# Performance work log

Measured on AMD Instinct MI355X. Metric: run time of the kernel, lower is better.

## Reference

```python
import jax, jax.numpy as jnp
import numpy as np

SEQ_LEN = 8192
DIM_AUD = 2048
NEG_SLOPE = 0.02


def _leaky(z):
    return jnp.where(z >= 0, z, NEG_SLOPE * z)


def _conv1d(x, w, b):
    # x: [1, Cin, L], w: [Cout, Cin, 3], b: [Cout]; stride 1, padding 1
    y = jax.lax.conv_general_dilated(
        x, w, window_strides=(1,), padding=[(1, 1)],
        dimension_numbers=('NCH', 'OIH', 'NCH'))
    return y + b[None, :, None]


def setup_inputs() -> dict:
    key = jax.random.key(0)
    ks = jax.random.split(key, 13)
    def rn(k, shape, fan_in):
        return jax.random.normal(k, shape, dtype=jnp.float32) * (1.0 / np.sqrt(fan_in))
    x = jax.random.normal(ks[0], (SEQ_LEN, DIM_AUD), dtype=jnp.float32)
    w1 = rn(ks[1], (16, DIM_AUD, 3), DIM_AUD * 3); b1 = jnp.zeros((16,), jnp.float32)
    w2 = rn(ks[2], (8, 16, 3), 16 * 3);            b2 = jnp.zeros((8,), jnp.float32)
    w3 = rn(ks[3], (4, 8, 3), 8 * 3);              b3 = jnp.zeros((4,), jnp.float32)
    w4 = rn(ks[4], (2, 4, 3), 4 * 3);              b4 = jnp.zeros((2,), jnp.float32)
    w5 = rn(ks[5], (1, 2, 3), 2 * 3);              b5 = jnp.zeros((1,), jnp.float32)
    Wl = rn(ks[6], (SEQ_LEN, SEQ_LEN), SEQ_LEN);   bl = jnp.zeros((SEQ_LEN,), jnp.float32)
    return {"x": x, "w1": w1, "b1": b1, "w2": w2, "b2": b2, "w3": w3, "b3": b3,
            "w4": w4, "b4": b4, "w5": w5, "b5": b5, "Wl": Wl, "bl": bl}


def reference(x, w1, b1, w2, b2, w3, b3, w4, b4, w5, b5, Wl, bl):
    # y: [1, dim_aud, seq_len]
    y = x[:, :DIM_AUD].T[None]
    y = _leaky(_conv1d(y, w1, b1))
    y = _leaky(_conv1d(y, w2, b2))
    y = _leaky(_conv1d(y, w3, b3))
    y = _leaky(_conv1d(y, w4, b4))
    y = _leaky(_conv1d(y, w5, b5))          # [1, 1, seq_len]
    logits = y.reshape(1, SEQ_LEN) @ Wl.T + bl  # torch Linear: x @ W.T + b
    att = jax.nn.softmax(logits, axis=1).reshape(SEQ_LEN, 1)
    return jnp.sum(att * x, axis=0)          # [dim_aud]
```

## Files before the change

kernel.cpp:

```cpp
#include <hip/hip_runtime.h>

#define SEQ 8192
#define DIM 2048
#define NEG 0.02f

__global__ __launch_bounds__(256, 2) void k_conv1(
    const float* __restrict__ x, const float* __restrict__ w1,
    float* __restrict__ out1p) {
  __shared__ float wlds[32 * 16 * 12];
  __shared__ float xs[32 * 260];

  const int tid = threadIdx.x;
  const int tb = blockIdx.x & 31;
  const int slice = blockIdx.x >> 5;
  const int cinb = slice * 128;

  for (int i = tid; i < 6144; i += 256) {
    int c = i / 384;
    int rem = i - c * 384;
    int uu = rem / 3;
    int k = rem - uu * 3;
    float v = w1[c * 6144 + (cinb + uu) * 3 + k];
    wlds[((uu >> 2) * 16 + c) * 12 + k * 4 + (uu & 3)] = v;
  }

  const int cg = tid & 3;
  const int tg = tid >> 2;
  const int qc = tid & 7;
  const int rs = tid >> 3;

  float acc[4][4];
  #pragma unroll
  for (int i = 0; i < 4; ++i)
    #pragma unroll
    for (int tt = 0; tt < 4; ++tt) acc[i][tt] = 0.f;

  const float4* x4 = (const float4*)x;

  for (int ch = 0; ch < 4; ++ch) {
    __syncthreads();
    #pragma unroll
    for (int it = 0; it < 9; ++it) {
      int r = rs + it * 32;
      if (r < 258) {
        int gt = tb * 256 - 1 + r;
        float4 v = make_float4(0.f, 0.f, 0.f, 0.f);
        if (gt >= 0 && gt < SEQ)
          v = x4[gt * 512 + (cinb >> 2) + ch * 8 + qc];
        xs[(4 * qc + 0) * 260 + r] = v.x;
        xs[(4 * qc + 1) * 260 + r] = v.y;
        xs[(4 * qc + 2) * 260 + r] = v.z;
        xs[(4 * qc + 3) * 260 + r] = v.w;
      }
    }
    __syncthreads();

    #pragma unroll 1
    for (int gg = 0; gg < 8; ++gg) {
      const float4* wp = (const float4*)&wlds[(ch * 8 + gg) * 16 * 12];
      float4 wk[4][3];
      #pragma unroll
      for (int i = 0; i < 4; ++i)
        #pragma unroll
        for (int k = 0; k < 3; ++k)
          wk[i][k] = wp[(4 * cg + i) * 3 + k];
      const float* wkf = (const float*)wk;

      #pragma unroll
      for (int u = 0; u < 4; ++u) {
        const float* xb = &xs[(gg * 4 + u) * 260 + 4 * tg];
        float4 xa = *(const float4*)xb;
        float2 xt = *(const float2*)(xb + 4);
        float xv[6] = {xa.x, xa.y, xa.z, xa.w, xt.x, xt.y};
        #pragma unroll
        for (int i = 0; i < 4; ++i) {
          #pragma unroll
          for (int k = 0; k < 3; ++k) {
            float wv = wkf[(i * 3 + k) * 4 + u];
            #pragma unroll
            for (int tt = 0; tt < 4; ++tt)
              acc[i][tt] += wv * xv[tt + k];
          }
        }
      }
    }
  }

  #pragma unroll
  for (int i = 0; i < 4; ++i) {
    float4 o = make_float4(acc[i][0], acc[i][1], acc[i][2], acc[i][3]);
    int c = 4 * cg + i;
    ((float4*)out1p)[(slice * 16 + c) * 2048 + tb * 64 + tg] = o;
  }
}

__global__ __launch_bounds__(128) void k_chain(
    const float* __restrict__ out1p, const float* __restrict__ b1,
    const float* __restrict__ w2, const float* __restrict__ b2,
    const float* __restrict__ w3, const float* __restrict__ b3,
    const float* __restrict__ w4, const float* __restrict__ b4,
    const float* __restrict__ w5, const float* __restrict__ b5,
    float* __restrict__ y5) {
  __shared__ float l1[16][72], l2[8][72], l3[4][72], l4[2][72];
  __shared__ float w2s[384], w3s[96], w4s[24], w5s[6];
  __shared__ float bs[16];

  const int tid = threadIdx.x;
  const int t0 = blockIdx.x * 64;

  for (int i = tid; i < 384; i += 128) w2s[i] = w2[i];
  if (tid < 96) w3s[tid] = w3[tid];
  else if (tid < 120) w4s[tid - 96] = w4[tid - 96];
  else if (tid == 120) { for (int i = 0; i < 6; ++i) w5s[i] = w5[i]; }
  else if (tid == 121) {
    for (int i = 0; i < 8; ++i) bs[i] = b2[i];
    for (int i = 0; i < 4; ++i) bs[8 + i] = b3[i];
    bs[12] = b4[0]; bs[13] = b4[1]; bs[14] = b5[0];
  }

  const float4* p4 = (const float4*)out1p;
  for (int idx = tid; idx < 16 * 18; idx += 128) {
    int cc = idx / 18, m = idx - cc * 18;
    int gt0 = t0 - 4 + 4 * m;
    float4 a = make_float4(0.f, 0.f, 0.f, 0.f);
    if (gt0 >= 0 && gt0 < SEQ) {
      int base = cc * 2048 + (gt0 >> 2);
      #pragma unroll
      for (int s = 0; s < 16; ++s) {
        float4 v = p4[s * 16 * 2048 + base];
        a.x += v.x; a.y += v.y; a.z += v.z; a.w += v.w;
      }
    }
    float bb = b1[cc];
    float e0 = a.x + bb, e1 = a.y + bb, e2 = a.z + bb, e3 = a.w + bb;
    l1[cc][4 * m + 0] = (e0 >= 0.f) ? e0 : NEG * e0;
    l1[cc][4 * m + 1] = (e1 >= 0.f) ? e1 : NEG * e1;
    l1[cc][4 * m + 2] = (e2 >= 0.f) ? e2 : NEG * e2;
    l1[cc][4 * m + 3] = (e3 >= 0.f) ? e3 : NEG * e3;
  }
  __syncthreads();

  for (int o = tid; o < 560; o += 128) {
    int j = (o >> 3) + 1, cc = o & 7;
    float acc = bs[cc];
    #pragma unroll
    for (int ci = 0; ci < 16; ++ci) {
      acc += w2s[cc * 48 + ci * 3 + 0] * l1[ci][j - 1];
      acc += w2s[cc * 48 + ci * 3 + 1] * l1[ci][j];
      acc += w2s[cc * 48 + ci * 3 + 2] * l1[ci][j + 1];
    }
    l2[cc][j] = (acc >= 0.f) ? acc : NEG * acc;
  }
  __syncthreads();

  for (int o = tid; o < 272; o += 128) {
    int j = (o >> 2) + 2, cc = o & 3;
    float acc = bs[8 + cc];
    #pragma unroll
    for (int ci = 0; ci < 8; ++ci) {
      acc += w3s[cc * 24 + ci * 3 + 0] * l2[ci][j - 1];
      acc += w3s[cc * 24 + ci * 3 + 1] * l2[ci][j];
      acc += w3s[cc * 24 + ci * 3 + 2] * l2[ci][j + 1];
    }
    l3[cc][j] = (acc >= 0.f) ? acc : NEG * acc;
  }
  __syncthreads();

  for (int o = tid; o < 132; o += 128) {
    int j = (o >> 1) + 3, cc = o & 1;
    float acc = bs[12 + cc];
    #pragma unroll
    for (int ci = 0; ci < 4; ++ci) {
      acc += w4s[cc * 12 + ci * 3 + 0] * l3[ci][j - 1];
      acc += w4s[cc * 12 + ci * 3 + 1] * l3[ci][j];
      acc += w4s[cc * 12 + ci * 3 + 2] * l3[ci][j + 1];
    }
    l4[cc][j] = (acc >= 0.f) ? acc : NEG * acc;
  }
  __syncthreads();

  for (int o = tid; o < 64; o += 128) {
    int j = o + 4;
    float acc = bs[14];
    #pragma unroll
    for (int ci = 0; ci < 2; ++ci) {
      acc += w5s[ci * 3 + 0] * l4[ci][j - 1];
      acc += w5s[ci * 3 + 1] * l4[ci][j];
      acc += w5s[ci * 3 + 2] * l4[ci][j + 1];
    }
    y5[t0 + o] = (acc >= 0.f) ? acc : NEG * acc;
  }
}

__global__ __launch_bounds__(256) void k_matvec(
    const float* __restrict__ Wl, const float* __restrict__ bl,
    const float* __restrict__ y5, float* __restrict__ logits) {
  const int tid = threadIdx.x;
  const int r0 = blockIdx.x * 8;
  const float4* W4 = (const float4*)Wl;
  const float4* y4 = (const float4*)y5;

  float a[8];
  #pragma unroll
  for (int r = 0; r < 8; ++r) a[r] = 0.f;

  #pragma unroll 2
  for (int u = 0; u < 8; ++u) {
    int i = u * 256 + tid;
    float4 yv = y4[i];
    #pragma unroll
    for (int r = 0; r < 8; ++r) {
      float4 wv = W4[(r0 + r) * 2048 + i];
      a[r] += wv.x * yv.x + wv.y * yv.y + wv.z * yv.z + wv.w * yv.w;
    }
  }
  #pragma unroll
  for (int o = 32; o; o >>= 1) {
    #pragma unroll
    for (int r = 0; r < 8; ++r) a[r] += __shfl_down(a[r], o);
  }
  __shared__ float red[4][8];
  const int lane = tid & 63, wid = tid >> 6;
  if (lane == 0) {
    #pragma unroll
    for (int r = 0; r < 8; ++r) red[wid][r] = a[r];
  }
  __syncthreads();
  if (tid < 8) {
    float s = red[0][tid] + red[1][tid] + red[2][tid] + red[3][tid];
    logits[r0 + tid] = s + bl[r0 + tid];
  }
}

__global__ __launch_bounds__(256) void k_stats(
    const float* __restrict__ logits, float* __restrict__ stats) {
  __shared__ float red[4];
  const int tid = threadIdx.x;
  const int lane = tid & 63, wid = tid >> 6;

  float lv[32];
  #pragma unroll
  for (int i = 0; i < 32; ++i) lv[i] = logits[tid + 256 * i];

  float m = lv[0];
  #pragma unroll
  for (int i = 1; i < 32; ++i) m = fmaxf(m, lv[i]);
  #pragma unroll
  for (int o = 32; o; o >>= 1) m = fmaxf(m, __shfl_down(m, o));
  if (lane == 0) red[wid] = m;
  __syncthreads();
  const float M = fmaxf(fmaxf(red[0], red[1]), fmaxf(red[2], red[3]));
  __syncthreads();

  float s = 0.f;
  #pragma unroll
  for (int i = 0; i < 32; ++i) s += __expf(lv[i] - M);
  #pragma unroll
  for (int o = 32; o; o >>= 1) s += __shfl_down(s, o);
  if (lane == 0) red[wid] = s;
  __syncthreads();
  if (tid == 0) {
    float S = red[0] + red[1] + red[2] + red[3];
    stats[0] = M;
    stats[1] = 1.0f / S;
  }
}

__global__ __launch_bounds__(256) void k_wsum(
    const float* __restrict__ x, const float* __restrict__ logits,
    const float* __restrict__ stats, float* __restrict__ partial) {
  const int tid = threadIdx.x;
  const int lane = tid & 63, wv = tid >> 6;
  const int tc = blockIdx.x >> 3, strip = blockIdx.x & 7;
  const float M = stats[0], invS = stats[1];
  const float4* x4 = (const float4*)x;
  const int col = strip * 64 + lane;
  const int t0 = tc * 64 + wv * 16;

  float4 acc = make_float4(0.f, 0.f, 0.f, 0.f);
  #pragma unroll 4
  for (int tt = 0; tt < 16; ++tt) {
    int t = t0 + tt;
    float a = __expf(logits[t] - M) * invS;
    float4 xv = x4[t * 512 + col];
    acc.x += a * xv.x; acc.y += a * xv.y; acc.z += a * xv.z; acc.w += a * xv.w;
  }

  __shared__ float4 redx[4][64];
  redx[wv][lane] = acc;
  __syncthreads();
  if (wv == 0) {
    float4 s = redx[0][lane];
    #pragma unroll
    for (int w = 1; w < 4; ++w) {
      float4 v = redx[w][lane];
      s.x += v.x; s.y += v.y; s.z += v.z; s.w += v.w;
    }
    ((float4*)partial)[tc * 512 + col] = s;
  }
}

__global__ __launch_bounds__(256) void k_reduce(
    const float* __restrict__ partial, float* __restrict__ out) {
  const int col = blockIdx.x * 256 + threadIdx.x;
  float s = 0.f;
  #pragma unroll 8
  for (int tc = 0; tc < 128; ++tc) s += partial[tc * 2048 + col];
  out[col] = s;
}

extern "C" void kernel_launch(void* const* d_in, const int* in_sizes, int n_in,
                              void* d_out, int out_size, void* d_ws, size_t ws_size,
                              hipStream_t stream) {
  const float* x  = (const float*)d_in[0];
  const float* w1 = (const float*)d_in[1];
  const float* b1 = (const float*)d_in[2];
  const float* w2 = (const float*)d_in[3];
  const float* b2 = (const float*)d_in[4];
  const float* w3 = (const float*)d_in[5];
  const float* b3 = (const float*)d_in[6];
  const float* w4 = (const float*)d_in[7];
  const float* b4 = (const float*)d_in[8];
  const float* w5 = (const float*)d_in[9];
  const float* b5 = (const float*)d_in[10];
  const float* Wl = (const float*)d_in[11];
  const float* bl = (const float*)d_in[12];
  float* out = (float*)d_out;

  float* ws      = (float*)d_ws;
  float* out1p   = ws;
  float* y5      = out1p + 16 * 16 * SEQ;
  float* logits  = y5 + SEQ;
  float* stats   = logits + SEQ;
  float* partial = stats + 16;

  k_conv1 <<<512, 256, 0, stream>>>(x, w1, out1p);
  k_chain <<<128, 128, 0, stream>>>(out1p, b1, w2, b2, w3, b3, w4, b4, w5, b5, y5);
  k_matvec<<<1024, 256, 0, stream>>>(Wl, bl, y5, logits);
  k_stats <<<1, 256, 0, stream>>>(logits, stats);
  k_wsum  <<<1024, 256, 0, stream>>>(x, logits, stats, partial);
  k_reduce<<<8, 256, 0, stream>>>(partial, out);
}
```

Before: 118.3 us.

## Pre-transpose conv1 weights and read them wave-uniformly from global memory

Adds a small prep kernel that repacks w1 into a [cin][cout] float4 layout, so each conv1 block no longer builds a weight tile in LDS. The conv1 thread mapping changes so each wave owns four output channels, which makes the weight loads wave-uniform and lets them come from scalar or cached global reads. The x tile in LDS gets per-row padding to avoid bank conflicts. The cost is an extra kernel launch and weight reads from global or L2 inside the inner loop.

After: 140.3 us. +18.6%, slower.

```diff
diff --git a/kernel.cpp b/kernel.cpp
--- a/kernel.cpp
+++ b/kernel.cpp
@@ -4,30 +4,35 @@
 #define DIM 2048
 #define NEG 0.02f
 
+__global__ __launch_bounds__(256) void k_prep(
+    const float* __restrict__ w1, float* __restrict__ wT) {
+  int i = blockIdx.x * 256 + threadIdx.x;
+  if (i < 32768) {
+    int cin = i >> 4, c = i & 15;
+    const float* s = w1 + c * 6144 + cin * 3;
+    ((float4*)wT)[i] = make_float4(s[0], s[1], s[2], 0.f);
+  }
+}
+
+__device__ __forceinline__ int row_off(int j) {
+  return j * 260 + (j >> 2) * 4;
+}
+
 __global__ __launch_bounds__(256, 2) void k_conv1(
-    const float* __restrict__ x, const float* __restrict__ w1,
+    const float* __restrict__ x, const float* __restrict__ wT,
     float* __restrict__ out1p) {
-  __shared__ float wlds[32 * 16 * 12];
-  __shared__ float xs[32 * 260];
+  __shared__ float xs[8348];
 
   const int tid = threadIdx.x;
   const int tb = blockIdx.x & 31;
   const int slice = blockIdx.x >> 5;
-  const int cinb = slice * 128;
-
-  for (int i = tid; i < 6144; i += 256) {
-    int c = i / 384;
-    int rem = i - c * 384;
-    int uu = rem / 3;
-    int k = rem - uu * 3;
-    float v = w1[c * 6144 + (cinb + uu) * 3 + k];
-    wlds[((uu >> 2) * 16 + c) * 12 + k * 4 + (uu & 3)] = v;
-  }
-
-  const int cg = tid & 3;
-  const int tg = tid >> 2;
+  const int cinb = slice << 7;
+  const int lane = tid & 63;
+  const int wv = __builtin_amdgcn_readfirstlane(tid >> 6);
+  const int t0 = tb << 8;
   const int qc = tid & 7;
   const int rs = tid >> 3;
+  const float4* x4 = (const float4*)x;
 
   float acc[4][4];
   #pragma unroll
@@ -35,53 +40,44 @@
     #pragma unroll
     for (int tt = 0; tt < 4; ++tt) acc[i][tt] = 0.f;
 
-  const float4* x4 = (const float4*)x;
+  const float* xrow = xs + (lane << 2);
 
   for (int ch = 0; ch < 4; ++ch) {
     __syncthreads();
     #pragma unroll
     for (int it = 0; it < 9; ++it) {
-      int r = rs + it * 32;
+      int r = rs + (it << 5);
       if (r < 258) {
-        int gt = tb * 256 - 1 + r;
+        int gt = t0 - 1 + r;
         float4 v = make_float4(0.f, 0.f, 0.f, 0.f);
         if (gt >= 0 && gt < SEQ)
-          v = x4[gt * 512 + (cinb >> 2) + ch * 8 + qc];
-        xs[(4 * qc + 0) * 260 + r] = v.x;
-        xs[(4 * qc + 1) * 260 + r] = v.y;
-        xs[(4 * qc + 2) * 260 + r] = v.z;
-        xs[(4 * qc + 3) * 260 + r] = v.w;
+          v = x4[gt * 512 + (cinb >> 2) + (ch << 3) + qc];
+        xs[row_off(4 * qc + 0) + r] = v.x;
+        xs[row_off(4 * qc + 1) + r] = v.y;
+        xs[row_off(4 * qc + 2) + r] = v.z;
+        xs[row_off(4 * qc + 3) + r] = v.w;
       }
     }
     __syncthreads();
 
-    #pragma unroll 1
-    for (int gg = 0; gg < 8; ++gg) {
-      const float4* wp = (const float4*)&wlds[(ch * 8 + gg) * 16 * 12];
-      float4 wk[4][3];
+    const float4* wq = ((const float4*)wT) + (((cinb + (ch << 5)) << 4) + (wv << 2));
+
+    #pragma unroll 8
+    for (int cin = 0; cin < 32; ++cin) {
+      float4 w0 = wq[(cin << 4) + 0];
+      float4 w1v = wq[(cin << 4) + 1];
+      float4 w2v = wq[(cin << 4) + 2];
+      float4 w3v = wq[(cin << 4) + 3];
+      const float* xb = xrow + row_off(cin);
+      float4 xa = *(const float4*)xb;
+      float2 xt = *(const float2*)(xb + 4);
+      float xv[6] = {xa.x, xa.y, xa.z, xa.w, xt.x, xt.y};
       #pragma unroll
-      for (int i = 0; i < 4; ++i)
-        #pragma unroll
-        for (int k = 0; k < 3; ++k)
-          wk[i][k] = wp[(4 * cg + i) * 3 + k];
-      const float* wkf = (const float*)wk;
-
-      #pragma unroll
-      for (int u = 0; u < 4; ++u) {
-        const float* xb = &xs[(gg * 4 + u) * 260 + 4 * tg];
-        float4 xa = *(const float4*)xb;
-        float2 xt = *(const float2*)(xb + 4);
-        float xv[6] = {xa.x, xa.y, xa.z, xa.w, xt.x, xt.y};
-        #pragma unroll
-        for (int i = 0; i < 4; ++i) {
-          #pragma unroll
-          for (int k = 0; k < 3; ++k) {
-            float wv = wkf[(i * 3 + k) * 4 + u];
-            #pragma unroll
-            for (int tt = 0; tt < 4; ++tt)
-              acc[i][tt] += wv * xv[tt + k];
-          }
-        }
+      for (int tt = 0; tt < 4; ++tt) {
+        acc[0][tt] += w0.x * xv[tt] + w0.y * xv[tt + 1] + w0.z * xv[tt + 2];
+        acc[1][tt] += w1v.x * xv[tt] + w1v.y * xv[tt + 1] + w1v.z * xv[tt + 2];
+        acc[2][tt] += w2v.x * xv[tt] + w2v.y * xv[tt + 1] + w2v.z * xv[tt + 2];
+        acc[3][tt] += w3v.x * xv[tt] + w3v.y * xv[tt + 1] + w3v.z * xv[tt + 2];
       }
     }
   }
@@ -89,8 +85,8 @@
   #pragma unroll
   for (int i = 0; i < 4; ++i) {
     float4 o = make_float4(acc[i][0], acc[i][1], acc[i][2], acc[i][3]);
-    int c = 4 * cg + i;
-    ((float4*)out1p)[(slice * 16 + c) * 2048 + tb * 64 + tg] = o;
+    int c = (wv << 2) + i;
+    ((float4*)out1p)[(slice * 16 + c) * 2048 + (t0 >> 2) + lane] = o;
   }
 }
 
@@ -328,13 +324,15 @@
   float* out = (float*)d_out;
 
   float* ws      = (float*)d_ws;
-  float* out1p   = ws;
+  float* wT      = ws;
+  float* out1p   = wT + 131072;
   float* y5      = out1p + 16 * 16 * SEQ;
   float* logits  = y5 + SEQ;
   float* stats   = logits + SEQ;
   float* partial = stats + 16;
 
-  k_conv1 <<<512, 256, 0, stream>>>(x, w1, out1p);
+  k_prep  <<<128, 256, 0, stream>>>(w1, wT);
+  k_conv1 <<<512, 256, 0, stream>>>(x, wT, out1p);
   k_chain <<<128, 128, 0, stream>>>(out1p, b1, w2, b2, w3, b3, w4, b4, w5, b5, y5);
   k_matvec<<<1024, 256, 0, stream>>>(Wl, bl, y5, logits);
   k_stats <<<1, 256, 0, stream>>>(logits, stats);
```

## Retile conv1 with wave-uniform output channels and padded LDS rows

Applied to the files above, without the earlier changes.

The first convolution is retiled so each block covers 512 time steps and 64 input channels, and each wave owns 4 output channels. Weights become wave-uniform, and each thread computes 8 time points. LDS rows get periodic padding to reduce bank conflicts, and the three taps are folded into one expression. The trade-off is twice as many partial slices (32 instead of 16), so the chain kernel reads a larger partial buffer and the workspace grows. Out-of-range halo entries in the chain kernel are now written as zero instead of leaky(bias).

Result: slower. 136.7 us (+15.5%).

```diff
diff --git a/kernel.cpp b/kernel.cpp
--- a/kernel.cpp
+++ b/kernel.cpp
@@ -4,82 +4,90 @@
 #define DIM 2048
 #define NEG 0.02f
 
+__device__ __forceinline__ int row_off(int j) {
+  return j * 520 + (j >> 2) * 4;
+}
+
 __global__ __launch_bounds__(256, 2) void k_conv1(
     const float* __restrict__ x, const float* __restrict__ w1,
     float* __restrict__ out1p) {
-  __shared__ float wlds[32 * 16 * 12];
-  __shared__ float xs[32 * 260];
-
-  const int tid = threadIdx.x;
-  const int tb = blockIdx.x & 31;
-  const int slice = blockIdx.x >> 5;
-  const int cinb = slice * 128;
-
-  for (int i = tid; i < 6144; i += 256) {
-    int c = i / 384;
-    int rem = i - c * 384;
-    int uu = rem / 3;
-    int k = rem - uu * 3;
-    float v = w1[c * 6144 + (cinb + uu) * 3 + k];
-    wlds[((uu >> 2) * 16 + c) * 12 + k * 4 + (uu & 3)] = v;
-  }
-
-  const int cg = tid & 3;
-  const int tg = tid >> 2;
-  const int qc = tid & 7;
-  const int rs = tid >> 3;
-
-  float acc[4][4];
+  __shared__ float wlds[16 * 16 * 12];
+  __shared__ float xs[8332];
+
+  const int tid = threadIdx.x;
+  const int tb = blockIdx.x & 15;
+  const int slice = blockIdx.x >> 4;
+  const int cinb = slice << 6;
+  const int lane = tid & 63;
+  const int wv = __builtin_amdgcn_readfirstlane(tid >> 6);
+  const int t0 = tb << 9;
+  const float4* x4 = (const float4*)x;
+
+  for (int i = tid; i < 3072; i += 256) {
+    int g = i / 192;
+    int rem = i - g * 192;
+    int c = rem / 12;
+    int m = rem - c * 12;
+    int k = m >> 2, u = m & 3;
+    wlds[i] = w1[c * 6144 + (cinb + 4 * g + u) * 3 + k];
+  }
+
+  float acc[4][8];
   #pragma unroll
   for (int i = 0; i < 4; ++i)
     #pragma unroll
-    for (int tt = 0; tt < 4; ++tt) acc[i][tt] = 0.f;
-
-  const float4* x4 = (const float4*)x;
+    for (int t = 0; t < 8; ++t) acc[i][t] = 0.f;
+
+  const int qc = tid & 3;
+  const int rsb = tid >> 2;
 
   for (int ch = 0; ch < 4; ++ch) {
     __syncthreads();
     #pragma unroll
     for (int it = 0; it < 9; ++it) {
-      int r = rs + it * 32;
-      if (r < 258) {
-        int gt = tb * 256 - 1 + r;
+      int srr = rsb + (it << 6);
+      if (srr < 516) {
+        int region = (srr >= 258) ? 1 : 0;
+        int rr = srr - 258 * region;
+        int gt = t0 - 1 + rr + (region << 8);
         float4 v = make_float4(0.f, 0.f, 0.f, 0.f);
         if (gt >= 0 && gt < SEQ)
-          v = x4[gt * 512 + (cinb >> 2) + ch * 8 + qc];
-        xs[(4 * qc + 0) * 260 + r] = v.x;
-        xs[(4 * qc + 1) * 260 + r] = v.y;
-        xs[(4 * qc + 2) * 260 + r] = v.z;
-        xs[(4 * qc + 3) * 260 + r] = v.w;
+          v = x4[gt * 512 + (cinb >> 2) + (ch << 2) + qc];
+        int base = region * 260 + rr;
+        xs[row_off(4 * qc + 0) + base] = v.x;
+        xs[row_off(4 * qc + 1) + base] = v.y;
+        xs[row_off(4 * qc + 2) + base] = v.z;
+        xs[row_off(4 * qc + 3) + base] = v.w;
       }
     }
     __syncthreads();
 
-    #pragma unroll 1
-    for (int gg = 0; gg < 8; ++gg) {
-      const float4* wp = (const float4*)&wlds[(ch * 8 + gg) * 16 * 12];
-      float4 wk[4][3];
+    #pragma unroll 2
+    for (int gg = 0; gg < 4; ++gg) {
+      const float4* wq = ((const float4*)wlds) +
+                         ((((ch << 2) + gg) * 16 + (wv << 2)) * 3);
+      float4 wk[12];
       #pragma unroll
-      for (int i = 0; i < 4; ++i)
-        #pragma unroll
-        for (int k = 0; k < 3; ++k)
-          wk[i][k] = wp[(4 * cg + i) * 3 + k];
+      for (int m = 0; m < 12; ++m) wk[m] = wq[m];
       const float* wkf = (const float*)wk;
 
       #pragma unroll
       for (int u = 0; u < 4; ++u) {
-        const float* xb = &xs[(gg * 4 + u) * 260 + 4 * tg];
-        float4 xa = *(const float4*)xb;
-        float2 xt = *(const float2*)(xb + 4);
-        float xv[6] = {xa.x, xa.y, xa.z, xa.w, xt.x, xt.y};
+        const float* xb = xs + row_off((gg << 2) + u) + (lane << 2);
         #pragma unroll
-        for (int i = 0; i < 4; ++i) {
+        for (int T = 0; T < 2; ++T) {
+          float4 xa = *(const float4*)(xb + 260 * T);
+          float2 xt = *(const float2*)(xb + 260 * T + 4);
+          float xv[6] = {xa.x, xa.y, xa.z, xa.w, xt.x, xt.y};
           #pragma unroll
-          for (int k = 0; k < 3; ++k) {
-            float wv = wkf[(i * 3 + k) * 4 + u];
+          for (int i = 0; i < 4; ++i) {
+            float w0 = wkf[(i * 3 + 0) * 4 + u];
+            float w1v = wkf[(i * 3 + 1) * 4 + u];
+            float w2v = wkf[(i * 3 + 2) * 4 + u];
             #pragma unroll
             for (int tt = 0; tt < 4; ++tt)
-              acc[i][tt] += wv * xv[tt + k];
+              acc[i][T * 4 + tt] +=
+                  w0 * xv[tt] + w1v * xv[tt + 1] + w2v * xv[tt + 2];
           }
         }
       }
@@ -88,9 +96,12 @@
 
   #pragma unroll
   for (int i = 0; i < 4; ++i) {
-    float4 o = make_float4(acc[i][0], acc[i][1], acc[i][2], acc[i][3]);
-    int c = 4 * cg + i;
-    ((float4*)out1p)[(slice * 16 + c) * 2048 + tb * 64 + tg] = o;
+    int c = (wv << 2) + i;
+    float4 o0 = make_float4(acc[i][0], acc[i][1], acc[i][2], acc[i][3]);
+    float4 o1 = make_float4(acc[i][4], acc[i][5], acc[i][6], acc[i][7]);
+    float4* dst = ((float4*)out1p) + (slice * 16 + c) * 2048 + (t0 >> 2);
+    dst[lane] = o0;
+    dst[64 + lane] = o1;
   }
 }
 
@@ -122,21 +133,24 @@
   for (int idx = tid; idx < 16 * 18; idx += 128) {
     int cc = idx / 18, m = idx - cc * 18;
     int gt0 = t0 - 4 + 4 * m;
-    float4 a = make_float4(0.f, 0.f, 0.f, 0.f);
     if (gt0 >= 0 && gt0 < SEQ) {
+      float4 a = make_float4(0.f, 0.f, 0.f, 0.f);
       int base = cc * 2048 + (gt0 >> 2);
-      #pragma unroll
-      for (int s = 0; s < 16; ++s) {
+      #pragma unroll 8
+      for (int s = 0; s < 32; ++s) {
         float4 v = p4[s * 16 * 2048 + base];
         a.x += v.x; a.y += v.y; a.z += v.z; a.w += v.w;
       }
-    }
-    float bb = b1[cc];
-    float e0 = a.x + bb, e1 = a.y + bb, e2 = a.z + bb, e3 = a.w + bb;
-    l1[cc][4 * m + 0] = (e0 >= 0.f) ? e0 : NEG * e0;
-    l1[cc][4 * m + 1] = (e1 >= 0.f) ? e1 : NEG * e1;
-    l1[cc][4 * m + 2] = (e2 >= 0.f) ? e2 : NEG * e2;
-    l1[cc][4 * m + 3] = (e3 >= 0.f) ? e3 : NEG * e3;
+      float bb = b1[cc];
+      float e0 = a.x + bb, e1 = a.y + bb, e2 = a.z + bb, e3 = a.w + bb;
+      l1[cc][4 * m + 0] = (e0 >= 0.f) ? e0 : NEG * e0;
+      l1[cc][4 * m + 1] = (e1 >= 0.f) ? e1 : NEG * e1;
+      l1[cc][4 * m + 2] = (e2 >= 0.f) ? e2 : NEG * e2;
+      l1[cc][4 * m + 3] = (e3 >= 0.f) ? e3 : NEG * e3;
+    } else {
+      l1[cc][4 * m + 0] = 0.f; l1[cc][4 * m + 1] = 0.f;
+      l1[cc][4 * m + 2] = 0.f; l1[cc][4 * m + 3] = 0.f;
+    }
   }
   __syncthreads();
 
@@ -329,7 +343,7 @@
 
   float* ws      = (float*)d_ws;
   float* out1p   = ws;
-  float* y5      = out1p + 16 * 16 * SEQ;
+  float* y5      = out1p + 32 * 16 * SEQ;
   float* logits  = y5 + SEQ;
   float* stats   = logits + SEQ;
   float* partial = stats + 16;
```
